# Optimization experiments

Measured on AMD Instinct MI355X. Metric: run time of the kernel, lower is better.

Reference implementation:

```python
import jax, jax.numpy as jnp
import numpy as np

N_PAIRS = 100000
N_TRIP = 500000
PAIR_DIM = 128
GEOM_DIM = 4


def _mlp(x, w1, b1, w2, b2):
    return jax.nn.silu(x @ w1 + b1) @ w2 + b2


def setup_inputs() -> dict:
    key = jax.random.key(0)
    ks = jax.random.split(key, 16)

    def lin(k, fan_in, fan_out):
        bound = 1.0 / np.sqrt(fan_in)
        kw, kb = jax.random.split(k)
        w = jax.random.uniform(kw, (fan_in, fan_out), jnp.float32, -bound, bound)
        b = jax.random.uniform(kb, (fan_out,), jnp.float32, -bound, bound)
        return w, b

    psi_w1, psi_b1 = lin(ks[0], 3 * PAIR_DIM + GEOM_DIM, PAIR_DIM)
    psi_w2, psi_b2 = lin(ks[1], PAIR_DIM, PAIR_DIM)
    phi_w1, phi_b1 = lin(ks[2], 2 * PAIR_DIM, PAIR_DIM)
    phi_w2, phi_b2 = lin(ks[3], PAIR_DIM, PAIR_DIM)

    return {
        "h_pair": jax.random.normal(ks[4], (N_PAIRS, PAIR_DIM), jnp.float32),
        "pair_vu_idx": jax.random.randint(ks[5], (N_TRIP,), 0, N_PAIRS, jnp.int64 if jax.config.jax_enable_x64 else jnp.int32).astype(jnp.int32),
        "pair_uw_idx": jax.random.randint(ks[6], (N_TRIP,), 0, N_PAIRS).astype(jnp.int32),
        "pair_vw_idx": jax.random.randint(ks[7], (N_TRIP,), 0, N_PAIRS).astype(jnp.int32),
        "geom_features": jax.random.normal(ks[8], (N_TRIP, GEOM_DIM), jnp.float32),
        "psi_w1": psi_w1, "psi_b1": psi_b1, "psi_w2": psi_w2, "psi_b2": psi_b2,
        "phi_w1": phi_w1, "phi_b1": phi_b1, "phi_w2": phi_w2, "phi_b2": phi_b2,
    }


def reference(h_pair, pair_vu_idx, pair_uw_idx, pair_vw_idx, geom_features,
              psi_w1, psi_b1, psi_w2, psi_b2,
              phi_w1, phi_b1, phi_w2, phi_b2):
    # gather triplet endpoints: [T, pair_dim] each
    h_vu = h_pair[pair_vu_idx]
    h_uw = h_pair[pair_uw_idx]
    h_vw = h_pair[pair_vw_idx]
    triplet_input = jnp.concatenate([h_vu, h_uw, h_vw, geom_features], axis=-1)  # [T, 3D+G]
    m_triplet = _mlp(triplet_input, psi_w1, psi_b1, psi_w2, psi_b2)  # [T, D]
    # scatter-add back onto pairs indexed by vw
    agg = jax.ops.segment_sum(m_triplet, pair_vw_idx, num_segments=h_pair.shape[0])  # [N, D]
    updated = _mlp(jnp.concatenate([h_pair, agg], axis=-1), phi_w1, phi_b1, phi_w2, phi_b2)
    return h_pair + updated
```

## Files before the change

### kernel.cpp

```cpp
#include <hip/hip_runtime.h>
#include <hip/hip_bf16.h>

#define T_TRIP 500000
#define NP     100000
#define NTILES 7813

typedef float f32x4 __attribute__((ext_vector_type(4)));
typedef __bf16 bf16x8 __attribute__((ext_vector_type(8)));
typedef unsigned short u16;
typedef unsigned short u16x8 __attribute__((ext_vector_type(8)));

__device__ __forceinline__ u16 f2bf(float f) {
  union { float f; unsigned u; } v; v.f = f;
  unsigned r = v.u + 0x7fffu + ((v.u >> 16) & 1u);
  return (u16)(r >> 16);
}

__device__ __forceinline__ ushort4 cvt4(float4 v) {
  ushort4 o; o.x = f2bf(v.x); o.y = f2bf(v.y); o.z = f2bf(v.z); o.w = f2bf(v.w);
  return o;
}

__device__ __forceinline__ u16 cvt1_pk(float v) {
  unsigned r;
  asm("v_cvt_pk_bf16_f32 %0, %1, %1" : "=v"(r) : "v"(v));
  return (u16)r;
}

#define MFMA16(a, b, c) __builtin_amdgcn_mfma_f32_16x16x32_bf16((a), (b), (c), 0, 0, 0)

#define WAITVM(N) asm volatile("s_waitcnt vmcnt(" #N ")" ::: "memory")
#define LGKM0()   asm volatile("s_waitcnt lgkmcnt(0)" ::: "memory")

__device__ __forceinline__ void barrier_raw() {
  asm volatile("" ::: "memory");
  __builtin_amdgcn_s_barrier();
  asm volatile("" ::: "memory");
  __builtin_amdgcn_sched_barrier(0);
}

__device__ __forceinline__ void gload_lds16(const u16* g, u16* l) {
  __builtin_amdgcn_global_load_lds((const __attribute__((address_space(1))) void*)g,
                                   (__attribute__((address_space(3))) void*)l, 16, 0, 0);
}
__device__ __forceinline__ void gload_lds4(const int* g, int* l) {
  __builtin_amdgcn_global_load_lds((const __attribute__((address_space(1))) void*)g,
                                   (__attribute__((address_space(3))) void*)l, 4, 0, 0);
}

#define FP_W1A   0u
#define FP_W1B   16384u
#define FP_W1C   32768u
#define FP_W2    49152u
#define FP_PW1   65536u
#define FP_PW2   98304u
#define FP_W1D   114688u
#define FP_H     131072u
#define FP_AGG   12931072u
#define WS_NEED_BYTES 51462144ull

#define HSTR  136
#define GSTR  520
#define X2STR 264

__global__ void k_prep_fast(const float* __restrict__ psi_w1, const float* __restrict__ psi_w2,
                            const float* __restrict__ phi_w1, const float* __restrict__ phi_w2,
                            u16* __restrict__ ws) {
  int i = blockIdx.x * 256 + threadIdx.x;
  if (i < 49152) {
    int s = i / 16384, r = i % 16384;
    int n = r / 128, k = r % 128;
    ws[FP_W1A + i] = f2bf(psi_w1[(s * 128 + k) * 128 + n]);
    return;
  }
  i -= 49152;
  if (i < 16384) {
    int n = i / 128, k = i % 128;
    ws[FP_W2 + i] = f2bf(psi_w2[k * 128 + n]);
    return;
  }
  i -= 16384;
  if (i < 32768) {
    int n = i / 256, k = i % 256;
    ws[FP_PW1 + i] = f2bf(phi_w1[k * 128 + n]);
    return;
  }
  i -= 32768;
  if (i < 16384) {
    int n = i / 128, k = i % 128;
    ws[FP_PW2 + i] = f2bf(phi_w2[k * 128 + n]);
    return;
  }
  i -= 16384;
  if (i < 512) {
    int k = i / 128, n = i % 128;
    reinterpret_cast<float*>(ws + FP_W1D)[i] = psi_w1[(384 + k) * 128 + n];
  }
}

__global__ void k_hconv(const float* __restrict__ h, u16* __restrict__ H, u16* __restrict__ AGG) {
  const size_t i = (size_t)(blockIdx.x * 256 + threadIdx.x) * 8;
  float4 v0 = *reinterpret_cast<const float4*>(h + i);
  float4 v1 = *reinterpret_cast<const float4*>(h + i + 4);
  *reinterpret_cast<ushort4*>(H + i)     = cvt4(v0);
  *reinterpret_cast<ushort4*>(H + i + 4) = cvt4(v1);
  ushort4 z = {0, 0, 0, 0};
  *reinterpret_cast<ushort4*>(AGG + i)     = z;
  *reinterpret_cast<ushort4*>(AGG + i + 4) = z;
}

__global__ __launch_bounds__(256, 3) void k_triplet_fast(
    const u16* __restrict__ H,
    const int* __restrict__ ivu, const int* __restrict__ iuw, const int* __restrict__ ivw,
    const float* __restrict__ geom,
    const u16* __restrict__ W1A, const u16* __restrict__ W1B, const u16* __restrict__ W1C,
    const float* __restrict__ w1dF, const u16* __restrict__ W2T,
    const float* __restrict__ b1, const float* __restrict__ b2,
    u16* __restrict__ AGG) {
  __shared__ __align__(16) u16 XB[2][16 * GSTR];
  __shared__ __align__(16) u16 hl[64 * HSTR];
  __shared__ __align__(16) float geomF[64][4];
  __shared__ __align__(16) int aIvu[2][64];
  __shared__ __align__(16) int aIuw[64];
  __shared__ __align__(16) int svw[2][64];

  const int tid = threadIdx.x;
  const int w = tid >> 6, l = tid & 63;
  const int lr = l & 15;
  const int lk = (l >> 4) << 3;
  const int n0 = w * 32 + lr;
  const int rowh = (l >> 4) << 2;
  const int srow = l >> 4;
  const int schunk = (l & 15) ^ ((l >> 4) << 1);

  bf16x8 w2f[4][2];
#pragma unroll
  for (int ks = 0; ks < 4; ++ks)
#pragma unroll
    for (int ct = 0; ct < 2; ++ct)
      w2f[ks][ct] = *reinterpret_cast<const bf16x8*>(&W2T[(size_t)(n0 + ct * 16) * 128 + ks * 32 + lk]);
  const float b1v[2] = {b1[n0], b1[n0 + 16]};
  const float b2v[2] = {b2[n0], b2[n0 + 16]};
  float w1dv[4][2];
#pragma unroll
  for (int k = 0; k < 4; ++k) {
    w1dv[k][0] = w1dF[k * 128 + n0];
    w1dv[k][1] = w1dF[k * 128 + n0 + 16];
  }

  auto stage_src_lds = [&](const int* idxL, int buf) {
#pragma unroll
    for (int q = 0; q < 4; ++q) {
      const int g = w * 4 + q;
      const int idx = idxL[g * 4 + srow];
      gload_lds16(H + (size_t)idx * 128 + schunk * 8, &XB[buf][g * GSTR]);
    }
  };

  auto stage_aux = [&](int tn, int tn2, int buf) {
    if (w == 0) {
      int t = tn2 * 64 + l; t = (t < T_TRIP) ? t : (T_TRIP - 1);
      gload_lds4(ivu + t, &aIvu[buf][0]);
    } else if (w == 1) {
      int t = tn * 64 + l; t = (t < T_TRIP) ? t : (T_TRIP - 1);
      gload_lds4(iuw + t, &aIuw[0]);
    } else if (w == 2) {
      int t = tn * 64 + l; t = (t < T_TRIP) ? t : (T_TRIP - 1);
      gload_lds4(ivw + t, &svw[buf][0]);
    } else {
      int t = tn * 64 + l; t = (t < T_TRIP) ? t : (T_TRIP - 1);
      gload_lds16(reinterpret_cast<const u16*>(geom + (size_t)t * 4),
                  reinterpret_cast<u16*>(&geomF[0][0]));
    }
  };

  auto gemm_src = [&](const u16* WT, int buf, f32x4 (&acc)[4][2]) {
#pragma unroll
    for (int ks = 0; ks < 4; ++ks) {
      bf16x8 a[4], b[2];
#pragma unroll
      for (int rt = 0; rt < 4; ++rt) {
        const int r = rt * 16 + lr;
        const int g = r >> 2, s = r & 3;
        const int j = ks * 4 + (l >> 4);
        a[rt] = *reinterpret_cast<const bf16x8*>(&XB[buf][g * GSTR + s * 128 + ((j ^ (s << 1)) << 3)]);
      }
#pragma unroll
      for (int ct = 0; ct < 2; ++ct)
        b[ct] = *reinterpret_cast<const bf16x8*>(&WT[(size_t)(n0 + ct * 16) * 128 + ks * 32 + lk]);
#pragma unroll
      for (int rt = 0; rt < 4; ++rt)
#pragma unroll
        for (int ct = 0; ct < 2; ++ct)
          acc[rt][ct] = MFMA16(a[rt], b[ct], acc[rt][ct]);
    }
  };

  int4 dst4[4];
  f32x4 acc2c[4][2];
#pragma unroll
  for (int rt = 0; rt < 4; ++rt) {
    dst4[rt] = make_int4(-1, -1, -1, -1);
#pragma unroll
    for (int ct = 0; ct < 2; ++ct) acc2c[rt][ct] = f32x4{0.f, 0.f, 0.f, 0.f};
  }

  auto scatter_prev = [&]() {
#pragma unroll
    for (int rt = 0; rt < 4; ++rt) {
#pragma unroll
      for (int j = 0; j < 4; ++j) {
        const int dst = (&dst4[rt].x)[j];
        float v0 = acc2c[rt][0][j];
        float v1 = acc2c[rt][1][j];
        float x0 = __shfl_xor(v0, 1);
        float x1 = __shfl_xor(v1, 1);
        const bool even = (l & 1) == 0;
        float lo = even ? v0 : x1;
        float hi = even ? x0 : v1;
        const int col = even ? n0 : (n0 + 15);
        if (dst >= 0) {
          u16* p = AGG + (size_t)dst * 128 + col;
          unsigned pk;
          asm("v_cvt_pk_bf16_f32 %0, %1, %2" : "=v"(pk) : "v"(lo), "v"(hi));
          asm volatile("global_atomic_pk_add_bf16 %0, %1, off" :: "v"(p), "v"(pk) : "memory");
        }
      }
    }
  };

  int pb = 0, tb = 0;
  int tt = blockIdx.x;
  const int G = gridDim.x;

  {
    int tn2 = (tt + G < NTILES) ? tt + G : tt;
    stage_aux(tt, tn2, 0);
#pragma unroll
    for (int q = 0; q < 4; ++q) {
      const int g = w * 4 + q;
      int t = tt * 64 + g * 4 + srow; t = (t < T_TRIP) ? t : (T_TRIP - 1);
      const int idx = ivu[t];
      gload_lds16(H + (size_t)idx * 128 + schunk * 8, &XB[0][g * GSTR]);
    }
    WAITVM(0);
    barrier_raw();
  }

  for (; tt < NTILES; tt += G) {
    const int t0 = tt * 64;

    stage_src_lds(aIuw, pb ^ 1);
    WAITVM(4);
    barrier_raw();

    f32x4 acc[4][2] = {};
    gemm_src(W1A, pb, acc);
    barrier_raw();

    int4 nd[4];
#pragma unroll
    for (int rt = 0; rt < 4; ++rt)
      nd[rt] = *reinterpret_cast<const int4*>(&svw[tb][rt * 16 + rowh]);
    stage_src_lds(&svw[tb][0], pb);
    WAITVM(4);
    barrier_raw();

    gemm_src(W1B, pb ^ 1, acc);
    WAITVM(0);
    barrier_raw();

    stage_src_lds(&aIvu[tb][0], pb ^ 1);

    gemm_src(W1C, pb, acc);

    scatter_prev();

#pragma unroll
    for (int rt = 0; rt < 4; ++rt)
#pragma unroll
      for (int j = 0; j < 4; ++j) {
        const float4 g4 = *reinterpret_cast<const float4*>(&geomF[rt * 16 + rowh + j][0]);
#pragma unroll
        for (int ct = 0; ct < 2; ++ct)
          acc[rt][ct][j] += g4.x * w1dv[0][ct] + g4.y * w1dv[1][ct] +
                            g4.z * w1dv[2][ct] + g4.w * w1dv[3][ct];
      }
#pragma unroll
    for (int rt = 0; rt < 4; ++rt)
#pragma unroll
      for (int ct = 0; ct < 2; ++ct) {
        const float bb = b1v[ct];
#pragma unroll
        for (int j = 0; j < 4; ++j) {
          float v = acc[rt][ct][j] + bb;
          v = v * __builtin_amdgcn_rcpf(1.f + __expf(-v));
          hl[(rt * 16 + rowh + j) * HSTR + n0 + ct * 16] = cvt1_pk(v);
        }
      }
    LGKM0();
    barrier_raw();

    {
      int tn = (tt + G < NTILES) ? tt + G : tt;
      int tn2 = (tt + 2 * G < NTILES) ? tt + 2 * G : tt;
      stage_aux(tn, tn2, tb ^ 1);
    }

    f32x4 acc2[4][2] = {};
#pragma unroll
    for (int ks = 0; ks < 4; ++ks) {
      bf16x8 a[4];
#pragma unroll
      for (int rt = 0; rt < 4; ++rt)
        a[rt] = *reinterpret_cast<const bf16x8*>(&hl[(rt * 16 + lr) * HSTR + ks * 32 + lk]);
#pragma unroll
      for (int rt = 0; rt < 4; ++rt)
#pragma unroll
        for (int ct = 0; ct < 2; ++ct)
          acc2[rt][ct] = MFMA16(a[rt], w2f[ks][ct], acc2[rt][ct]);
    }

#pragma unroll
    for (int rt = 0; rt < 4; ++rt) {
#pragma unroll
      for (int j = 0; j < 4; ++j) {
        const int trow = t0 + rt * 16 + rowh + j;
        (&dst4[rt].x)[j] = (trow < T_TRIP) ? (&nd[rt].x)[j] : -1;
      }
#pragma unroll
      for (int ct = 0; ct < 2; ++ct)
        acc2c[rt][ct] = acc2[rt][ct] + b2v[ct];
    }

    WAITVM(0);
    barrier_raw();
    pb ^= 1; tb ^= 1;
  }

  scatter_prev();
  WAITVM(0);
}

__global__ __launch_bounds__(256, 3) void k_pair_fast(
    const float* __restrict__ h_pair, const u16* __restrict__ H, const u16* __restrict__ AGG,
    const u16* __restrict__ PW1T, const u16* __restrict__ PW2T,
    const float* __restrict__ b1, const float* __restrict__ b2,
    float* __restrict__ out) {
  __shared__ __align__(16) u16 xl[64 * X2STR];
  __shared__ __align__(16) u16 hl[64 * HSTR];

  const int tid = threadIdx.x;
  const int r0 = blockIdx.x * 64;

  {
    const int row = tid >> 2, q = tid & 3;
    int rc = r0 + row; rc = (rc < NP) ? rc : (NP - 1);
    const u16x8* sh = reinterpret_cast<const u16x8*>(H + (size_t)rc * 128 + q * 32);
    const u16x8* sa = reinterpret_cast<const u16x8*>(AGG + (size_t)rc * 128 + q * 32);
    u16x8* d1 = reinterpret_cast<u16x8*>(&xl[row * X2STR + q * 32]);
    u16x8* d2 = reinterpret_cast<u16x8*>(&xl[row * X2STR + 128 + q * 32]);
#pragma unroll
    for (int i = 0; i < 4; ++i) { d1[i] = sh[i]; d2[i] = sa[i]; }
  }
  __syncthreads();

  const int w = tid >> 6, l = tid & 63;
  const int lr = l & 15;
  const int lk = (l >> 4) << 3;
  const int n0 = w * 32 + lr;
  const int rowh = (l >> 4) << 2;

  f32x4 acc[4][2] = {};
#pragma unroll 1
  for (int ks = 0; ks < 8; ++ks) {
    const int k0 = ks * 32;
    bf16x8 a[4], b[2];
#pragma unroll
    for (int rt = 0; rt < 4; ++rt)
      a[rt] = *reinterpret_cast<const bf16x8*>(&xl[(rt * 16 + lr) * X2STR + k0 + lk]);
#pragma unroll
    for (int ct = 0; ct < 2; ++ct)
      b[ct] = *reinterpret_cast<const bf16x8*>(&PW1T[(size_t)(n0 + ct * 16) * 256 + k0 + lk]);
#pragma unroll
    for (int rt = 0; rt < 4; ++rt)
#pragma unroll
      for (int ct = 0; ct < 2; ++ct)
        acc[rt][ct] = MFMA16(a[rt], b[ct], acc[rt][ct]);
  }

  {
    const float b1v0 = b1[n0], b1v1 = b1[n0 + 16];
#pragma unroll
    for (int rt = 0; rt < 4; ++rt)
#pragma unroll
      for (int ct = 0; ct < 2; ++ct) {
        const float bb = ct ? b1v1 : b1v0;
#pragma unroll
        for (int j = 0; j < 4; ++j) {
          float v = acc[rt][ct][j] + bb;
          v = v * __builtin_amdgcn_rcpf(1.f + __expf(-v));
          hl[(rt * 16 + rowh + j) * HSTR + n0 + ct * 16] = cvt1_pk(v);
        }
      }
  }
  __syncthreads();

  f32x4 acc2[4][2] = {};
#pragma unroll
  for (int ks = 0; ks < 4; ++ks) {
    const int k0 = ks * 32;
    bf16x8 a[4], b[2];
#pragma unroll
    for (int rt = 0; rt < 4; ++rt)
      a[rt] = *reinterpret_cast<const bf16x8*>(&hl[(rt * 16 + lr) * HSTR + k0 + lk]);
#pragma unroll
    for (int ct = 0; ct < 2; ++ct)
      b[ct] = *reinterpret_cast<const bf16x8*>(&PW2T[(size_t)(n0 + ct * 16) * 128 + k0 + lk]);
#pragma unroll
    for (int rt = 0; rt < 4; ++rt)
#pragma unroll
      for (int ct = 0; ct < 2; ++ct)
        acc2[rt][ct] = MFMA16(a[rt], b[ct], acc2[rt][ct]);
  }

  {
    const float b2v0 = b2[n0], b2v1 = b2[n0 + 16];
#pragma unroll
    for (int rt = 0; rt < 4; ++rt)
#pragma unroll
      for (int j = 0; j < 4; ++j) {
        const int row = rt * 16 + rowh + j;
        const int r = r0 + row;
        if (r < NP) {
          out[(size_t)r * 128 + n0]      = h_pair[(size_t)r * 128 + n0]      + acc2[rt][0][j] + b2v0;
          out[(size_t)r * 128 + n0 + 16] = h_pair[(size_t)r * 128 + n0 + 16] + acc2[rt][1][j] + b2v1;
        }
      }
  }
}

#define PSI_W1T_OFF 0
#define PSI_W2T_OFF 53248
#define PHI_W1T_OFF 69632
#define PHI_W2T_OFF 102400
#define WS_U16_TOTAL 118784
#define XSTR 424

__global__ void k_prep(const float* __restrict__ psi_w1, const float* __restrict__ psi_w2,
                       const float* __restrict__ phi_w1, const float* __restrict__ phi_w2,
                       u16* __restrict__ ws) {
  int i = blockIdx.x * 256 + threadIdx.x;
  if (i < 128 * 416) {
    int n = i / 416, k = i % 416;
    ws[PSI_W1T_OFF + i] = f2bf(k < 388 ? psi_w1[k * 128 + n] : 0.f);
    return;
  }
  i -= 128 * 416;
  if (i < 128 * 128) {
    int n = i / 128, k = i % 128;
    ws[PSI_W2T_OFF + i] = f2bf(psi_w2[k * 128 + n]);
    return;
  }
  i -= 128 * 128;
  if (i < 128 * 256) {
    int n = i / 256, k = i % 256;
    ws[PHI_W1T_OFF + i] = f2bf(phi_w1[k * 128 + n]);
    return;
  }
  i -= 128 * 256;
  if (i < 128 * 128) {
    int n = i / 128, k = i % 128;
    ws[PHI_W2T_OFF + i] = f2bf(phi_w2[k * 128 + n]);
  }
}

__global__ __launch_bounds__(256, 2) void k_triplet(
    const float* __restrict__ h_pair,
    const int* __restrict__ ivu, const int* __restrict__ iuw, const int* __restrict__ ivw,
    const float* __restrict__ geom,
    const u16* __restrict__ W1T, const u16* __restrict__ W2T,
    const float* __restrict__ b1, const float* __restrict__ b2,
    float* __restrict__ agg) {
  __shared__ __align__(16) u16 xl[64 * XSTR];
  __shared__ __align__(16) u16 hl[64 * HSTR];
  __shared__ int svw[64];

  const int tid = threadIdx.x;
  const int t0 = blockIdx.x * 64;

  {
    const int row = tid >> 2, q = tid & 3;
    const int t = t0 + row;
    const int tc = (t < T_TRIP) ? t : (T_TRIP - 1);
    if (q == 0) svw[row] = (t < T_TRIP) ? ivw[tc] : -1;
    int idx[3];
    idx[0] = ivu[tc]; idx[1] = iuw[tc]; idx[2] = ivw[tc];
#pragma unroll
    for (int s = 0; s < 3; ++s) {
      const float4* src = reinterpret_cast<const float4*>(h_pair + (size_t)idx[s] * 128 + q * 32);
      u16* dst = &xl[row * XSTR + s * 128 + q * 32];
#pragma unroll
      for (int i = 0; i < 8; ++i)
        *reinterpret_cast<ushort4*>(dst + i * 4) = cvt4(src[i]);
    }
  }
  if (tid < 64) {
    const int t = t0 + tid;
    const int tc = (t < T_TRIP) ? t : (T_TRIP - 1);
    const float4 g = reinterpret_cast<const float4*>(geom)[tc];
    u16* dst = &xl[tid * XSTR + 384];
    *reinterpret_cast<ushort4*>(dst) = cvt4(g);
    ushort4 z = {0, 0, 0, 0};
#pragma unroll
    for (int i = 1; i < 8; ++i) *reinterpret_cast<ushort4*>(dst + i * 4) = z;
  }
  __syncthreads();

  const int w = tid >> 6;
  const int l = tid & 63;
  const int lr = l & 15;
  const int lk = (l >> 4) << 3;
  const int n0 = w * 32 + lr;
  const int rowh = (l >> 4) << 2;

  f32x4 acc[4][2] = {};
#pragma unroll 1
  for (int ks = 0; ks < 13; ++ks) {
    const int k0 = ks * 32;
    bf16x8 a[4], b[2];
#pragma unroll
    for (int rt = 0; rt < 4; ++rt)
      a[rt] = *reinterpret_cast<const bf16x8*>(&xl[(rt * 16 + lr) * XSTR + k0 + lk]);
#pragma unroll
    for (int ct = 0; ct < 2; ++ct)
      b[ct] = *reinterpret_cast<const bf16x8*>(&W1T[(size_t)(n0 + ct * 16) * 416 + k0 + lk]);
#pragma unroll
    for (int rt = 0; rt < 4; ++rt)
#pragma unroll
      for (int ct = 0; ct < 2; ++ct)
        acc[rt][ct] = MFMA16(a[rt], b[ct], acc[rt][ct]);
  }

  {
    const float b1v0 = b1[n0], b1v1 = b1[n0 + 16];
#pragma unroll
    for (int rt = 0; rt < 4; ++rt)
#pragma unroll
      for (int ct = 0; ct < 2; ++ct) {
        const float bb = ct ? b1v1 : b1v0;
#pragma unroll
        for (int j = 0; j < 4; ++j) {
          float v = acc[rt][ct][j] + bb;
          v = v / (1.f + __expf(-v));
          hl[(rt * 16 + rowh + j) * HSTR + n0 + ct * 16] = f2bf(v);
        }
      }
  }
  __syncthreads();

  f32x4 acc2[4][2] = {};
#pragma unroll
  for (int ks = 0; ks < 4; ++ks) {
    const int k0 = ks * 32;
    bf16x8 a[4], b[2];
#pragma unroll
    for (int rt = 0; rt < 4; ++rt)
      a[rt] = *reinterpret_cast<const bf16x8*>(&hl[(rt * 16 + lr) * HSTR + k0 + lk]);
#pragma unroll
    for (int ct = 0; ct < 2; ++ct)
      b[ct] = *reinterpret_cast<const bf16x8*>(&W2T[(size_t)(n0 + ct * 16) * 128 + k0 + lk]);
#pragma unroll
    for (int rt = 0; rt < 4; ++rt)
#pragma unroll
      for (int ct = 0; ct < 2; ++ct)
        acc2[rt][ct] = MFMA16(a[rt], b[ct], acc2[rt][ct]);
  }

  {
    const float b2v0 = b2[n0], b2v1 = b2[n0 + 16];
#pragma unroll
    for (int rt = 0; rt < 4; ++rt)
#pragma unroll
      for (int j = 0; j < 4; ++j) {
        const int row = rt * 16 + rowh + j;
        const int dst = svw[row];
        if (dst >= 0) {
          unsafeAtomicAdd(&agg[(size_t)dst * 128 + n0], acc2[rt][0][j] + b2v0);
          unsafeAtomicAdd(&agg[(size_t)dst * 128 + n0 + 16], acc2[rt][1][j] + b2v1);
        }
      }
  }
}

__global__ __launch_bounds__(256, 2) void k_pair(
    const float* __restrict__ h_pair,
    const u16* __restrict__ W1T, const u16* __restrict__ W2T,
    const float* __restrict__ b1, const float* __restrict__ b2,
    float* __restrict__ out) {
  __shared__ __align__(16) u16 xl[64 * X2STR];
  __shared__ __align__(16) u16 hl[64 * HSTR];

  const int tid = threadIdx.x;
  const int r0 = blockIdx.x * 64;

  {
    const int row = tid >> 2, q = tid & 3;
    const int r = r0 + row;
    const int rc = (r < NP) ? r : (NP - 1);
    const float4* s1 = reinterpret_cast<const float4*>(h_pair + (size_t)rc * 128 + q * 32);
    const float4* s2 = reinterpret_cast<const float4*>(out + (size_t)rc * 128 + q * 32);
    u16* d1 = &xl[row * X2STR + q * 32];
    u16* d2 = &xl[row * X2STR + 128 + q * 32];
#pragma unroll
    for (int i = 0; i < 8; ++i) {
      *reinterpret_cast<ushort4*>(d1 + i * 4) = cvt4(s1[i]);
      *reinterpret_cast<ushort4*>(d2 + i * 4) = cvt4(s2[i]);
    }
  }
  __syncthreads();

  const int w = tid >> 6;
  const int l = tid & 63;
  const int lr = l & 15;
  const int lk = (l >> 4) << 3;
  const int n0 = w * 32 + lr;
  const int rowh = (l >> 4) << 2;

  f32x4 acc[4][2] = {};
#pragma unroll 1
  for (int ks = 0; ks < 8; ++ks) {
    const int k0 = ks * 32;
    bf16x8 a[4], b[2];
#pragma unroll
    for (int rt = 0; rt < 4; ++rt)
      a[rt] = *reinterpret_cast<const bf16x8*>(&xl[(rt * 16 + lr) * X2STR + k0 + lk]);
#pragma unroll
    for (int ct = 0; ct < 2; ++ct)
      b[ct] = *reinterpret_cast<const bf16x8*>(&W1T[(size_t)(n0 + ct * 16) * 256 + k0 + lk]);
#pragma unroll
    for (int rt = 0; rt < 4; ++rt)
#pragma unroll
      for (int ct = 0; ct < 2; ++ct)
        acc[rt][ct] = MFMA16(a[rt], b[ct], acc[rt][ct]);
  }

  {
    const float b1v0 = b1[n0], b1v1 = b1[n0 + 16];
#pragma unroll
    for (int rt = 0; rt < 4; ++rt)
#pragma unroll
      for (int ct = 0; ct < 2; ++ct) {
        const float bb = ct ? b1v1 : b1v0;
#pragma unroll
        for (int j = 0; j < 4; ++j) {
          float v = acc[rt][ct][j] + bb;
          v = v / (1.f + __expf(-v));
          hl[(rt * 16 + rowh + j) * HSTR + n0 + ct * 16] = f2bf(v);
        }
      }
  }
  __syncthreads();

  f32x4 acc2[4][2] = {};
#pragma unroll
  for (int ks = 0; ks < 4; ++ks) {
    const int k0 = ks * 32;
    bf16x8 a[4], b[2];
#pragma unroll
    for (int rt = 0; rt < 4; ++rt)
      a[rt] = *reinterpret_cast<const bf16x8*>(&hl[(rt * 16 + lr) * HSTR + k0 + lk]);
#pragma unroll
    for (int ct = 0; ct < 2; ++ct)
      b[ct] = *reinterpret_cast<const bf16x8*>(&W2T[(size_t)(n0 + ct * 16) * 128 + k0 + lk]);
#pragma unroll
    for (int rt = 0; rt < 4; ++rt)
#pragma unroll
      for (int ct = 0; ct < 2; ++ct)
        acc2[rt][ct] = MFMA16(a[rt], b[ct], acc2[rt][ct]);
  }

  {
    const float b2v0 = b2[n0], b2v1 = b2[n0 + 16];
#pragma unroll
    for (int rt = 0; rt < 4; ++rt)
#pragma unroll
      for (int j = 0; j < 4; ++j) {
        const int row = rt * 16 + rowh + j;
        const int r = r0 + row;
        if (r < NP) {
          out[(size_t)r * 128 + n0]      = h_pair[(size_t)r * 128 + n0]      + acc2[rt][0][j] + b2v0;
          out[(size_t)r * 128 + n0 + 16] = h_pair[(size_t)r * 128 + n0 + 16] + acc2[rt][1][j] + b2v1;
        }
      }
  }
}

extern "C" void kernel_launch(void* const* d_in, const int* in_sizes, int n_in,
                              void* d_out, int out_size, void* d_ws, size_t ws_size,
                              hipStream_t stream) {
  const float* h_pair = (const float*)d_in[0];
  const int* ivu = (const int*)d_in[1];
  const int* iuw = (const int*)d_in[2];
  const int* ivw = (const int*)d_in[3];
  const float* geom = (const float*)d_in[4];
  const float* psi_w1 = (const float*)d_in[5];
  const float* psi_b1 = (const float*)d_in[6];
  const float* psi_w2 = (const float*)d_in[7];
  const float* psi_b2 = (const float*)d_in[8];
  const float* phi_w1 = (const float*)d_in[9];
  const float* phi_b1 = (const float*)d_in[10];
  const float* phi_w2 = (const float*)d_in[11];
  const float* phi_b2 = (const float*)d_in[12];

  float* out = (float*)d_out;
  u16* ws = (u16*)d_ws;

  if (ws_size >= WS_NEED_BYTES) {
    k_prep_fast<<<450, 256, 0, stream>>>(psi_w1, psi_w2, phi_w1, phi_w2, ws);
    k_hconv<<<6250, 256, 0, stream>>>(h_pair, ws + FP_H, ws + FP_AGG);
    k_triplet_fast<<<768, 256, 0, stream>>>(
        ws + FP_H, ivu, iuw, ivw, geom,
        ws + FP_W1A, ws + FP_W1B, ws + FP_W1C,
        reinterpret_cast<const float*>(ws + FP_W1D), ws + FP_W2,
        psi_b1, psi_b2, ws + FP_AGG);
    k_pair_fast<<<(NP + 63) / 64, 256, 0, stream>>>(
        h_pair, ws + FP_H, ws + FP_AGG,
        ws + FP_PW1, ws + FP_PW2, phi_b1, phi_b2, out);
  } else {
    hipMemsetAsync(d_out, 0, (size_t)out_size * sizeof(float), stream);
    k_prep<<<(WS_U16_TOTAL + 255) / 256, 256, 0, stream>>>(psi_w1, psi_w2, phi_w1, phi_w2, ws);
    k_triplet<<<(T_TRIP + 63) / 64, 256, 0, stream>>>(
        h_pair, ivu, iuw, ivw, geom,
        ws + PSI_W1T_OFF, ws + PSI_W2T_OFF, psi_b1, psi_b2, out);
    k_pair<<<(NP + 63) / 64, 256, 0, stream>>>(
        h_pair, ws + PHI_W1T_OFF, ws + PHI_W2T_OFF, phi_b1, phi_b2, out);
  }
}
```

Before: 299.3 us.

## Sort triplets by destination pair and replace atomic scatter with pull reduction

Adds a counting sort of triplets by their vw index (histogram, three-stage scan, atomic-cursor permutation), after which the triplet MLP writes per-triplet messages in bf16 to a dense buffer instead of issuing bf16 atomic adds. The pair kernel then sums each pair's contiguous message range before its MLP, so the scatter becomes segmented and contention-free. This trades the atomic traffic for several extra launches, a message buffer of about 128 MB written and read back, and a serial per-pair summation loop. The path only runs when the workspace is large enough. The old fast triplet kernel is also reworked to load indices directly rather than staging them in LDS.

New measurement: 408.7 us. 1.37x slower.

```diff
diff --git a/kernel.cpp b/kernel.cpp
--- a/kernel.cpp
+++ b/kernel.cpp
@@ -4,11 +4,13 @@
 #define T_TRIP 500000
 #define NP     100000
 #define NTILES 7813
+#define NPAD   500032
 
 typedef float f32x4 __attribute__((ext_vector_type(4)));
 typedef __bf16 bf16x8 __attribute__((ext_vector_type(8)));
 typedef unsigned short u16;
 typedef unsigned short u16x8 __attribute__((ext_vector_type(8)));
+typedef unsigned int u32;
 
 __device__ __forceinline__ u16 f2bf(float f) {
   union { float f; unsigned u; } v; v.f = f;
@@ -25,6 +27,13 @@
   unsigned r;
   asm("v_cvt_pk_bf16_f32 %0, %1, %1" : "=v"(r) : "v"(v));
   return (u16)r;
+}
+
+__device__ __forceinline__ float bflo(u32 d) {
+  union { u32 u; float f; } v; v.u = d << 16; return v.f;
+}
+__device__ __forceinline__ float bfhi(u32 d) {
+  union { u32 u; float f; } v; v.u = d & 0xffff0000u; return v.f;
 }
 
 #define MFMA16(a, b, c) __builtin_amdgcn_mfma_f32_16x16x32_bf16((a), (b), (c), 0, 0, 0)
@@ -59,6 +68,17 @@
 #define FP_AGG   12931072u
 #define WS_NEED_BYTES 51462144ull
 
+#define FP_M_BYTE 25862144ull
+#define SB_CNT    153870336ull
+#define SB_START  154270464ull
+#define SB_CURSOR 154670592ull
+#define SB_BSUM   155070720ull
+#define SB_IVU    155071232ull
+#define SB_IUW    157071360ull
+#define SB_IVW    159071488ull
+#define SB_GEOM   161071616ull
+#define WS_SORT_BYTES 169072128ull
+
 #define HSTR  136
 #define GSTR  520
 #define X2STR 264
@@ -107,6 +127,397 @@
   ushort4 z = {0, 0, 0, 0};
   *reinterpret_cast<ushort4*>(AGG + i)     = z;
   *reinterpret_cast<ushort4*>(AGG + i + 4) = z;
+}
+
+__global__ void k_hconv2(const float* __restrict__ h, u16* __restrict__ H) {
+  const size_t i = (size_t)(blockIdx.x * 256 + threadIdx.x) * 8;
+  float4 v0 = *reinterpret_cast<const float4*>(h + i);
+  float4 v1 = *reinterpret_cast<const float4*>(h + i + 4);
+  *reinterpret_cast<ushort4*>(H + i)     = cvt4(v0);
+  *reinterpret_cast<ushort4*>(H + i + 4) = cvt4(v1);
+}
+
+__global__ void k_hist(const int* __restrict__ ivw, int* __restrict__ cnt) {
+  int i = blockIdx.x * 256 + threadIdx.x;
+  if (i < T_TRIP) atomicAdd(&cnt[ivw[i]], 1);
+}
+
+__global__ __launch_bounds__(1024) void k_scan1(const int* __restrict__ cnt,
+                                                int* __restrict__ tmp, int* __restrict__ bsum) {
+  __shared__ int wsum[16];
+  const int idx = blockIdx.x * 1024 + threadIdx.x;
+  const int lane = threadIdx.x & 63, wid = threadIdx.x >> 6;
+  int v = (idx < NP) ? cnt[idx] : 0;
+  int x = v;
+#pragma unroll
+  for (int off = 1; off < 64; off <<= 1) {
+    int n = __shfl_up(x, off);
+    if (lane >= off) x += n;
+  }
+  if (lane == 63) wsum[wid] = x;
+  __syncthreads();
+  if (threadIdx.x < 16) {
+    int s = wsum[threadIdx.x];
+#pragma unroll
+    for (int off = 1; off < 16; off <<= 1) {
+      int n = __shfl_up(s, off);
+      if (threadIdx.x >= off) s += n;
+    }
+    wsum[threadIdx.x] = s;
+  }
+  __syncthreads();
+  const int base = wid ? wsum[wid - 1] : 0;
+  if (idx < NP) tmp[idx] = base + x - v;
+  if (threadIdx.x == 1023) bsum[blockIdx.x] = base + x;
+}
+
+__global__ void k_scan2(int* __restrict__ bsum) {
+  __shared__ int s[128];
+  const int t = threadIdx.x;
+  int v = (t < 98) ? bsum[t] : 0;
+  s[t] = v; __syncthreads();
+#pragma unroll
+  for (int off = 1; off < 128; off <<= 1) {
+    int a = (t >= off) ? s[t - off] : 0;
+    __syncthreads();
+    s[t] += a;
+    __syncthreads();
+  }
+  if (t < 98) bsum[t] = s[t] - v;
+}
+
+__global__ void k_scan3(const int* __restrict__ bsum, int* __restrict__ start,
+                        int* __restrict__ cursor) {
+  int idx = blockIdx.x * 256 + threadIdx.x;
+  if (idx < NP) {
+    int f = start[idx] + bsum[idx >> 10];
+    start[idx] = f;
+    cursor[idx] = f;
+  }
+  if (idx == 0) start[NP] = T_TRIP;
+}
+
+__global__ void k_perm(const int* __restrict__ ivu, const int* __restrict__ iuw,
+                       const int* __restrict__ ivw, const float* __restrict__ geom,
+                       int* __restrict__ cursor,
+                       int* __restrict__ ivu_s, int* __restrict__ iuw_s,
+                       int* __restrict__ ivw_s, float4* __restrict__ geom_s) {
+  int i = blockIdx.x * 256 + threadIdx.x;
+  if (i < T_TRIP) {
+    int v = ivw[i];
+    int pos = atomicAdd(&cursor[v], 1);
+    ivu_s[pos] = ivu[i];
+    iuw_s[pos] = iuw[i];
+    ivw_s[pos] = v;
+    geom_s[pos] = reinterpret_cast<const float4*>(geom)[i];
+  } else if (i < NPAD) {
+    ivu_s[i] = 0; iuw_s[i] = 0; ivw_s[i] = 0;
+    geom_s[i] = make_float4(0.f, 0.f, 0.f, 0.f);
+  }
+}
+
+__global__ __launch_bounds__(256, 3) void k_triplet_sorted(
+    const u16* __restrict__ H,
+    const int* __restrict__ ivu_s, const int* __restrict__ iuw_s, const int* __restrict__ ivw_s,
+    const float* __restrict__ geom_s,
+    const u16* __restrict__ W1A, const u16* __restrict__ W1B, const u16* __restrict__ W1C,
+    const float* __restrict__ w1dF, const u16* __restrict__ W2T,
+    const float* __restrict__ b1, const float* __restrict__ b2,
+    u32* __restrict__ M32) {
+  __shared__ __align__(16) u16 XB[2][16 * GSTR];
+  __shared__ __align__(16) u16 hl[64 * HSTR];
+  __shared__ __align__(16) float geomF[64][4];
+  __shared__ __align__(16) int aIvu[2][64];
+  __shared__ __align__(16) int aIuw[64];
+  __shared__ __align__(16) int aIvw[64];
+
+  const int tid = threadIdx.x;
+  const int w = tid >> 6, l = tid & 63;
+  const int lr = l & 15;
+  const int lk = (l >> 4) << 3;
+  const int n0 = w * 32 + lr;
+  const int rowh = (l >> 4) << 2;
+  const int srow = l >> 4;
+  const int schunk = (l & 15) ^ ((l >> 4) << 1);
+
+  bf16x8 w2f[4][2];
+#pragma unroll
+  for (int ks = 0; ks < 4; ++ks)
+#pragma unroll
+    for (int ct = 0; ct < 2; ++ct)
+      w2f[ks][ct] = *reinterpret_cast<const bf16x8*>(&W2T[(size_t)(n0 + ct * 16) * 128 + ks * 32 + lk]);
+  const float b1v[2] = {b1[n0], b1[n0 + 16]};
+  const float b2v[2] = {b2[n0], b2[n0 + 16]};
+  float w1dv[4][2];
+#pragma unroll
+  for (int k = 0; k < 4; ++k) {
+    w1dv[k][0] = w1dF[k * 128 + n0];
+    w1dv[k][1] = w1dF[k * 128 + n0 + 16];
+  }
+
+  auto stage_src_lds = [&](const int* idxL, int buf) {
+#pragma unroll
+    for (int q = 0; q < 4; ++q) {
+      const int g = w * 4 + q;
+      const int idx = idxL[g * 4 + srow];
+      gload_lds16(H + (size_t)idx * 128 + schunk * 8, &XB[buf][g * GSTR]);
+    }
+  };
+
+  auto stage_aux = [&](int tA, int tB, int buf) {
+    if (w == 0) {
+      gload_lds4(ivu_s + tB * 64 + l, &aIvu[buf][0]);
+    } else if (w == 1) {
+      gload_lds4(iuw_s + tA * 64 + l, &aIuw[0]);
+    } else if (w == 2) {
+      gload_lds4(ivw_s + tA * 64 + l, &aIvw[0]);
+    } else {
+      gload_lds16(reinterpret_cast<const u16*>(geom_s + (size_t)(tA * 64 + l) * 4),
+                  reinterpret_cast<u16*>(&geomF[0][0]));
+    }
+  };
+
+  auto gemm_src = [&](const u16* WT, int buf, f32x4 (&acc)[4][2]) {
+#pragma unroll
+    for (int ks = 0; ks < 4; ++ks) {
+      bf16x8 a[4], b[2];
+#pragma unroll
+      for (int rt = 0; rt < 4; ++rt) {
+        const int r = rt * 16 + lr;
+        const int g = r >> 2, s = r & 3;
+        const int j = ks * 4 + (l >> 4);
+        a[rt] = *reinterpret_cast<const bf16x8*>(&XB[buf][g * GSTR + s * 128 + ((j ^ (s << 1)) << 3)]);
+      }
+#pragma unroll
+      for (int ct = 0; ct < 2; ++ct)
+        b[ct] = *reinterpret_cast<const bf16x8*>(&WT[(size_t)(n0 + ct * 16) * 128 + ks * 32 + lk]);
+#pragma unroll
+      for (int rt = 0; rt < 4; ++rt)
+#pragma unroll
+        for (int ct = 0; ct < 2; ++ct)
+          acc[rt][ct] = MFMA16(a[rt], b[ct], acc[rt][ct]);
+    }
+  };
+
+  int pb = 0, tb = 0;
+  int tt = blockIdx.x;
+  const int G = gridDim.x;
+
+  {
+    int tB = (tt + G < NTILES) ? tt + G : NTILES - 1;
+    stage_aux(tt, tB, 0);
+#pragma unroll
+    for (int q = 0; q < 4; ++q) {
+      const int g = w * 4 + q;
+      const int t = tt * 64 + g * 4 + srow;
+      const int idx = ivu_s[t];
+      gload_lds16(H + (size_t)idx * 128 + schunk * 8, &XB[0][g * GSTR]);
+    }
+    WAITVM(0);
+    barrier_raw();
+  }
+
+  for (; tt < NTILES; tt += G) {
+    const int t0 = tt * 64;
+
+    stage_src_lds(aIuw, pb ^ 1);
+    f32x4 acc[4][2] = {};
+    gemm_src(W1A, pb, acc);
+    barrier_raw();
+
+    stage_src_lds(aIvw, pb);
+    WAITVM(4);
+    barrier_raw();
+
+    gemm_src(W1B, pb ^ 1, acc);
+    WAITVM(0);
+    barrier_raw();
+
+    stage_src_lds(&aIvu[tb][0], pb ^ 1);
+    gemm_src(W1C, pb, acc);
+
+#pragma unroll
+    for (int rt = 0; rt < 4; ++rt)
+#pragma unroll
+      for (int j = 0; j < 4; ++j) {
+        const float4 g4 = *reinterpret_cast<const float4*>(&geomF[rt * 16 + rowh + j][0]);
+#pragma unroll
+        for (int ct = 0; ct < 2; ++ct)
+          acc[rt][ct][j] += g4.x * w1dv[0][ct] + g4.y * w1dv[1][ct] +
+                            g4.z * w1dv[2][ct] + g4.w * w1dv[3][ct];
+      }
+#pragma unroll
+    for (int rt = 0; rt < 4; ++rt)
+#pragma unroll
+      for (int ct = 0; ct < 2; ++ct) {
+        const float bb = b1v[ct];
+#pragma unroll
+        for (int j = 0; j < 4; ++j) {
+          float v = acc[rt][ct][j] + bb;
+          v = v * __builtin_amdgcn_rcpf(1.f + __expf(-v));
+          hl[(rt * 16 + rowh + j) * HSTR + n0 + ct * 16] = cvt1_pk(v);
+        }
+      }
+    LGKM0();
+    barrier_raw();
+
+    {
+      int tA = (tt + G < NTILES) ? tt + G : NTILES - 1;
+      int tB = (tt + 2 * G < NTILES) ? tt + 2 * G : NTILES - 1;
+      stage_aux(tA, tB, tb ^ 1);
+    }
+
+    f32x4 acc2[4][2] = {};
+#pragma unroll
+    for (int ks = 0; ks < 4; ++ks) {
+      bf16x8 a[4];
+#pragma unroll
+      for (int rt = 0; rt < 4; ++rt)
+        a[rt] = *reinterpret_cast<const bf16x8*>(&hl[(rt * 16 + lr) * HSTR + ks * 32 + lk]);
+#pragma unroll
+      for (int rt = 0; rt < 4; ++rt)
+#pragma unroll
+        for (int ct = 0; ct < 2; ++ct)
+          acc2[rt][ct] = MFMA16(a[rt], w2f[ks][ct], acc2[rt][ct]);
+    }
+
+#pragma unroll
+    for (int rt = 0; rt < 4; ++rt)
+#pragma unroll
+      for (int j = 0; j < 4; ++j) {
+        float v0 = acc2[rt][0][j] + b2v[0];
+        float v1 = acc2[rt][1][j] + b2v[1];
+        float x0 = __shfl_xor(v0, 1);
+        float x1 = __shfl_xor(v1, 1);
+        const bool even = (l & 1) == 0;
+        float lo = even ? v0 : x1;
+        float hi = even ? x0 : v1;
+        const int dcol = even ? (n0 >> 1) : ((n0 + 15) >> 1);
+        u32 pk;
+        asm("v_cvt_pk_bf16_f32 %0, %1, %2" : "=v"(pk) : "v"(lo), "v"(hi));
+        const int row = t0 + rt * 16 + rowh + j;
+        M32[(size_t)row * 64 + dcol] = pk;
+      }
+
+    WAITVM(16);
+    barrier_raw();
+    pb ^= 1; tb ^= 1;
+  }
+  WAITVM(0);
+}
+
+__global__ __launch_bounds__(256, 3) void k_pair_pull(
+    const float* __restrict__ h_pair, const u16* __restrict__ H,
+    const u32* __restrict__ M32, const int* __restrict__ start,
+    const u16* __restrict__ PW1T, const u16* __restrict__ PW2T,
+    const float* __restrict__ b1, const float* __restrict__ b2,
+    float* __restrict__ out) {
+  __shared__ __align__(16) u16 xl[64 * X2STR];
+  __shared__ __align__(16) u16 hl[64 * HSTR];
+
+  const int tid = threadIdx.x;
+  const int r0 = blockIdx.x * 64;
+
+  {
+    const int row = tid >> 2, q = tid & 3;
+    int rc = r0 + row; rc = (rc < NP) ? rc : (NP - 1);
+    const u16x8* sh = reinterpret_cast<const u16x8*>(H + (size_t)rc * 128 + q * 32);
+    u16x8* d1 = reinterpret_cast<u16x8*>(&xl[row * X2STR + q * 32]);
+#pragma unroll
+    for (int i = 0; i < 4; ++i) d1[i] = sh[i];
+  }
+
+  const int w = tid >> 6, l = tid & 63;
+  u32* xl32 = reinterpret_cast<u32*>(xl);
+
+  for (int i = 0; i < 16; ++i) {
+    int p = r0 + w * 16 + i;
+    int pc = (p < NP) ? p : (NP - 1);
+    const int s = start[pc], e = start[pc + 1];
+    float lo = 0.f, hi = 0.f;
+    for (int r = s; r < e; ++r) {
+      u32 d = M32[(size_t)r * 64 + l];
+      lo += bflo(d);
+      hi += bfhi(d);
+    }
+    u32 pk;
+    asm("v_cvt_pk_bf16_f32 %0, %1, %2" : "=v"(pk) : "v"(lo), "v"(hi));
+    xl32[(w * 16 + i) * (X2STR / 2) + 64 + l] = pk;
+  }
+  __syncthreads();
+
+  const int lr = l & 15;
+  const int lk = (l >> 4) << 3;
+  const int n0 = w * 32 + lr;
+  const int rowh = (l >> 4) << 2;
+
+  f32x4 acc[4][2] = {};
+#pragma unroll 1
+  for (int ks = 0; ks < 8; ++ks) {
+    const int k0 = ks * 32;
+    bf16x8 a[4], b[2];
+#pragma unroll
+    for (int rt = 0; rt < 4; ++rt)
+      a[rt] = *reinterpret_cast<const bf16x8*>(&xl[(rt * 16 + lr) * X2STR + k0 + lk]);
+#pragma unroll
+    for (int ct = 0; ct < 2; ++ct)
+      b[ct] = *reinterpret_cast<const bf16x8*>(&PW1T[(size_t)(n0 + ct * 16) * 256 + k0 + lk]);
+#pragma unroll
+    for (int rt = 0; rt < 4; ++rt)
+#pragma unroll
+      for (int ct = 0; ct < 2; ++ct)
+        acc[rt][ct] = MFMA16(a[rt], b[ct], acc[rt][ct]);
+  }
+
+  {
+    const float b1v0 = b1[n0], b1v1 = b1[n0 + 16];
+#pragma unroll
+    for (int rt = 0; rt < 4; ++rt)
+#pragma unroll
+      for (int ct = 0; ct < 2; ++ct) {
+        const float bb = ct ? b1v1 : b1v0;
+#pragma unroll
+        for (int j = 0; j < 4; ++j) {
+          float v = acc[rt][ct][j] + bb;
+          v = v * __builtin_amdgcn_rcpf(1.f + __expf(-v));
+          hl[(rt * 16 + rowh + j) * HSTR + n0 + ct * 16] = cvt1_pk(v);
+        }
+      }
+  }
+  __syncthreads();
+
+  f32x4 acc2[4][2] = {};
+#pragma unroll
+  for (int ks = 0; ks < 4; ++ks) {
+    const int k0 = ks * 32;
+    bf16x8 a[4], b[2];
+#pragma unroll
+    for (int rt = 0; rt < 4; ++rt)
+      a[rt] = *reinterpret_cast<const bf16x8*>(&hl[(rt * 16 + lr) * HSTR + k0 + lk]);
+#pragma unroll
+    for (int ct = 0; ct < 2; ++ct)
+      b[ct] = *reinterpret_cast<const bf16x8*>(&PW2T[(size_t)(n0 + ct * 16) * 128 + k0 + lk]);
+#pragma unroll
+    for (int rt = 0; rt < 4; ++rt)
+#pragma unroll
+      for (int ct = 0; ct < 2; ++ct)
+        acc2[rt][ct] = MFMA16(a[rt], b[ct], acc2[rt][ct]);
+  }
+
+  {
+    const float b2v0 = b2[n0], b2v1 = b2[n0 + 16];
+#pragma unroll
+    for (int rt = 0; rt < 4; ++rt)
+#pragma unroll
+      for (int j = 0; j < 4; ++j) {
+        const int row = rt * 16 + rowh + j;
+        const int r = r0 + row;
+        if (r < NP) {
+          out[(size_t)r * 128 + n0]      = h_pair[(size_t)r * 128 + n0]      + acc2[rt][0][j] + b2v0;
+          out[(size_t)r * 128 + n0 + 16] = h_pair[(size_t)r * 128 + n0 + 16] + acc2[rt][1][j] + b2v1;
+        }
+      }
+  }
 }
 
 __global__ __launch_bounds__(256, 3) void k_triplet_fast(
@@ -119,10 +530,8 @@
     u16* __restrict__ AGG) {
   __shared__ __align__(16) u16 XB[2][16 * GSTR];
   __shared__ __align__(16) u16 hl[64 * HSTR];
-  __shared__ __align__(16) float geomF[64][4];
-  __shared__ __align__(16) int aIvu[2][64];
-  __shared__ __align__(16) int aIuw[64];
-  __shared__ __align__(16) int svw[2][64];
+  __shared__ __align__(16) float geomF[2][64][4];
+  __shared__ int svw[2][64];
 
   const int tid = threadIdx.x;
   const int w = tid >> 6, l = tid & 63;
@@ -148,29 +557,24 @@
     w1dv[k][1] = w1dF[k * 128 + n0 + 16];
   }
 
-  auto stage_src_lds = [&](const int* idxL, int buf) {
+  auto stage_src = [&](const int* idxa, int tile, int buf) {
+    const int t0 = tile * 64;
 #pragma unroll
     for (int q = 0; q < 4; ++q) {
       const int g = w * 4 + q;
-      const int idx = idxL[g * 4 + srow];
+      int t = t0 + g * 4 + srow; t = (t < T_TRIP) ? t : (T_TRIP - 1);
+      const int idx = idxa[t];
       gload_lds16(H + (size_t)idx * 128 + schunk * 8, &XB[buf][g * GSTR]);
     }
   };
 
-  auto stage_aux = [&](int tn, int tn2, int buf) {
+  auto stage_aux = [&](int tile, int tb2) {
+    int t = tile * 64 + l; t = (t < T_TRIP) ? t : (T_TRIP - 1);
     if (w == 0) {
-      int t = tn2 * 64 + l; t = (t < T_TRIP) ? t : (T_TRIP - 1);
-      gload_lds4(ivu + t, &aIvu[buf][0]);
+      gload_lds16(reinterpret_cast<const u16*>(geom + (size_t)t * 4),
+                  reinterpret_cast<u16*>(&geomF[tb2][0][0]));
     } else if (w == 1) {
-      int t = tn * 64 + l; t = (t < T_TRIP) ? t : (T_TRIP - 1);
-      gload_lds4(iuw + t, &aIuw[0]);
-    } else if (w == 2) {
-      int t = tn * 64 + l; t = (t < T_TRIP) ? t : (T_TRIP - 1);
-      gload_lds4(ivw + t, &svw[buf][0]);
-    } else {
-      int t = tn * 64 + l; t = (t < T_TRIP) ? t : (T_TRIP - 1);
-      gload_lds16(reinterpret_cast<const u16*>(geom + (size_t)t * 4),
-                  reinterpret_cast<u16*>(&geomF[0][0]));
+      gload_lds4(ivw + t, &svw[tb2][0]);
     }
   };
 
@@ -196,149 +600,103 @@
     }
   };
 
-  int4 dst4[4];
-  f32x4 acc2c[4][2];
-#pragma unroll
-  for (int rt = 0; rt < 4; ++rt) {
-    dst4[rt] = make_int4(-1, -1, -1, -1);
-#pragma unroll
-    for (int ct = 0; ct < 2; ++ct) acc2c[rt][ct] = f32x4{0.f, 0.f, 0.f, 0.f};
-  }
-
-  auto scatter_prev = [&]() {
+  int pb = 0, tb = 0;
+  int tt = blockIdx.x;
+  stage_src(ivu, tt, 0);
+
+  for (; tt < NTILES; tt += gridDim.x) {
+    const int t0 = tt * 64;
+    int ttn = tt + gridDim.x; if (ttn >= NTILES) ttn = tt;
+
+    stage_src(iuw, tt, pb ^ 1);
+    stage_aux(tt, tb);
+    WAITVM(4);
+    barrier_raw();
+
+    f32x4 acc[4][2] = {};
+    gemm_src(W1A, pb, acc);
+    barrier_raw();
+
+    stage_src(ivw, tt, pb);
+    WAITVM(4);
+    barrier_raw();
+
+    gemm_src(W1B, pb ^ 1, acc);
+    WAITVM(0);
+    barrier_raw();
+
+    stage_src(ivu, ttn, pb ^ 1);
+    gemm_src(W1C, pb, acc);
+
+#pragma unroll
+    for (int rt = 0; rt < 4; ++rt)
+#pragma unroll
+      for (int j = 0; j < 4; ++j) {
+        const float4 g4 = *reinterpret_cast<const float4*>(&geomF[tb][rt * 16 + rowh + j][0]);
+#pragma unroll
+        for (int ct = 0; ct < 2; ++ct)
+          acc[rt][ct][j] += g4.x * w1dv[0][ct] + g4.y * w1dv[1][ct] +
+                            g4.z * w1dv[2][ct] + g4.w * w1dv[3][ct];
+      }
+#pragma unroll
+    for (int rt = 0; rt < 4; ++rt)
+#pragma unroll
+      for (int ct = 0; ct < 2; ++ct) {
+        const float bb = b1v[ct];
+#pragma unroll
+        for (int j = 0; j < 4; ++j) {
+          float v = acc[rt][ct][j] + bb;
+          v = v * __builtin_amdgcn_rcpf(1.f + __expf(-v));
+          hl[(rt * 16 + rowh + j) * HSTR + n0 + ct * 16] = cvt1_pk(v);
+        }
+      }
+    LGKM0();
+    barrier_raw();
+
+    {
+      int tn = tt + gridDim.x; if (tn >= NTILES) tn = tt;
+      stage_aux(tn, tb ^ 1);
+    }
+
+    f32x4 acc2[4][2] = {};
+#pragma unroll
+    for (int ks = 0; ks < 4; ++ks) {
+      bf16x8 a[4];
+#pragma unroll
+      for (int rt = 0; rt < 4; ++rt)
+        a[rt] = *reinterpret_cast<const bf16x8*>(&hl[(rt * 16 + lr) * HSTR + ks * 32 + lk]);
+#pragma unroll
+      for (int rt = 0; rt < 4; ++rt)
+#pragma unroll
+        for (int ct = 0; ct < 2; ++ct)
+          acc2[rt][ct] = MFMA16(a[rt], w2f[ks][ct], acc2[rt][ct]);
+    }
+
 #pragma unroll
     for (int rt = 0; rt < 4; ++rt) {
+      const int4 d4 = *reinterpret_cast<const int4*>(&svw[tb][rt * 16 + rowh]);
 #pragma unroll
       for (int j = 0; j < 4; ++j) {
-        const int dst = (&dst4[rt].x)[j];
-        float v0 = acc2c[rt][0][j];
-        float v1 = acc2c[rt][1][j];
+        const int dst = (&d4.x)[j];
+        const int trow = t0 + rt * 16 + rowh + j;
+        float v0 = acc2[rt][0][j] + b2v[0];
+        float v1 = acc2[rt][1][j] + b2v[1];
         float x0 = __shfl_xor(v0, 1);
         float x1 = __shfl_xor(v1, 1);
         const bool even = (l & 1) == 0;
         float lo = even ? v0 : x1;
         float hi = even ? x0 : v1;
         const int col = even ? n0 : (n0 + 15);
-        if (dst >= 0) {
+        if (trow < T_TRIP) {
           u16* p = AGG + (size_t)dst * 128 + col;
-          unsigned pk;
+          u32 pk;
           asm("v_cvt_pk_bf16_f32 %0, %1, %2" : "=v"(pk) : "v"(lo), "v"(hi));
           asm volatile("global_atomic_pk_add_bf16 %0, %1, off" :: "v"(p), "v"(pk) : "memory");
         }
       }
     }
-  };
-
-  int pb = 0, tb = 0;
-  int tt = blockIdx.x;
-  const int G = gridDim.x;
-
-  {
-    int tn2 = (tt + G < NTILES) ? tt + G : tt;
-    stage_aux(tt, tn2, 0);
-#pragma unroll
-    for (int q = 0; q < 4; ++q) {
-      const int g = w * 4 + q;
-      int t = tt * 64 + g * 4 + srow; t = (t < T_TRIP) ? t : (T_TRIP - 1);
-      const int idx = ivu[t];
-      gload_lds16(H + (size_t)idx * 128 + schunk * 8, &XB[0][g * GSTR]);
-    }
-    WAITVM(0);
-    barrier_raw();
-  }
-
-  for (; tt < NTILES; tt += G) {
-    const int t0 = tt * 64;
-
-    stage_src_lds(aIuw, pb ^ 1);
-    WAITVM(4);
-    barrier_raw();
-
-    f32x4 acc[4][2] = {};
-    gemm_src(W1A, pb, acc);
-    barrier_raw();
-
-    int4 nd[4];
-#pragma unroll
-    for (int rt = 0; rt < 4; ++rt)
-      nd[rt] = *reinterpret_cast<const int4*>(&svw[tb][rt * 16 + rowh]);
-    stage_src_lds(&svw[tb][0], pb);
-    WAITVM(4);
-    barrier_raw();
-
-    gemm_src(W1B, pb ^ 1, acc);
-    WAITVM(0);
-    barrier_raw();
-
-    stage_src_lds(&aIvu[tb][0], pb ^ 1);
-
-    gemm_src(W1C, pb, acc);
-
-    scatter_prev();
-
-#pragma unroll
-    for (int rt = 0; rt < 4; ++rt)
-#pragma unroll
-      for (int j = 0; j < 4; ++j) {
-        const float4 g4 = *reinterpret_cast<const float4*>(&geomF[rt * 16 + rowh + j][0]);
-#pragma unroll
-        for (int ct = 0; ct < 2; ++ct)
-          acc[rt][ct][j] += g4.x * w1dv[0][ct] + g4.y * w1dv[1][ct] +
-                            g4.z * w1dv[2][ct] + g4.w * w1dv[3][ct];
-      }
-#pragma unroll
-    for (int rt = 0; rt < 4; ++rt)
-#pragma unroll
-      for (int ct = 0; ct < 2; ++ct) {
-        const float bb = b1v[ct];
-#pragma unroll
-        for (int j = 0; j < 4; ++j) {
-          float v = acc[rt][ct][j] + bb;
-          v = v * __builtin_amdgcn_rcpf(1.f + __expf(-v));
-          hl[(rt * 16 + rowh + j) * HSTR + n0 + ct * 16] = cvt1_pk(v);
-        }
-      }
-    LGKM0();
-    barrier_raw();
-
-    {
-      int tn = (tt + G < NTILES) ? tt + G : tt;
-      int tn2 = (tt + 2 * G < NTILES) ? tt + 2 * G : tt;
-      stage_aux(tn, tn2, tb ^ 1);
-    }
-
-    f32x4 acc2[4][2] = {};
-#pragma unroll
-    for (int ks = 0; ks < 4; ++ks) {
-      bf16x8 a[4];
-#pragma unroll
-      for (int rt = 0; rt < 4; ++rt)
-        a[rt] = *reinterpret_cast<const bf16x8*>(&hl[(rt * 16 + lr) * HSTR + ks * 32 + lk]);
-#pragma unroll
-      for (int rt = 0; rt < 4; ++rt)
-#pragma unroll
-        for (int ct = 0; ct < 2; ++ct)
-          acc2[rt][ct] = MFMA16(a[rt], w2f[ks][ct], acc2[rt][ct]);
-    }
-
-#pragma unroll
-    for (int rt = 0; rt < 4; ++rt) {
-#pragma unroll
-      for (int j = 0; j < 4; ++j) {
-        const int trow = t0 + rt * 16 + rowh + j;
-        (&dst4[rt].x)[j] = (trow < T_TRIP) ? (&nd[rt].x)[j] : -1;
-      }
-#pragma unroll
-      for (int ct = 0; ct < 2; ++ct)
-        acc2c[rt][ct] = acc2[rt][ct] + b2v[ct];
-    }
-
-    WAITVM(0);
-    barrier_raw();
     pb ^= 1; tb ^= 1;
   }
-
-  scatter_prev();
   WAITVM(0);
 }
 
@@ -715,8 +1073,37 @@
 
   float* out = (float*)d_out;
   u16* ws = (u16*)d_ws;
-
-  if (ws_size >= WS_NEED_BYTES) {
+  char* wsb = (char*)d_ws;
+
+  if (ws_size >= WS_SORT_BYTES) {
+    u32*  M32    = (u32*)(wsb + FP_M_BYTE);
+    int*  cnt    = (int*)(wsb + SB_CNT);
+    int*  start  = (int*)(wsb + SB_START);
+    int*  cursor = (int*)(wsb + SB_CURSOR);
+    int*  bsum   = (int*)(wsb + SB_BSUM);
+    int*  ivu_s  = (int*)(wsb + SB_IVU);
+    int*  iuw_s  = (int*)(wsb + SB_IUW);
+    int*  ivw_s  = (int*)(wsb + SB_IVW);
+    float4* geom_s = (float4*)(wsb + SB_GEOM);
+
+    k_prep_fast<<<450, 256, 0, stream>>>(psi_w1, psi_w2, phi_w1, phi_w2, ws);
+    k_hconv2<<<6250, 256, 0, stream>>>(h_pair, ws + FP_H);
+    hipMemsetAsync(cnt, 0, NP * sizeof(int), stream);
+    k_hist<<<(T_TRIP + 255) / 256, 256, 0, stream>>>(ivw, cnt);
+    k_scan1<<<98, 1024, 0, stream>>>(cnt, start, bsum);
+    k_scan2<<<1, 128, 0, stream>>>(bsum);
+    k_scan3<<<(NP + 255) / 256, 256, 0, stream>>>(bsum, start, cursor);
+    k_perm<<<(NPAD + 255) / 256, 256, 0, stream>>>(ivu, iuw, ivw, geom, cursor,
+                                                   ivu_s, iuw_s, ivw_s, geom_s);
+    k_triplet_sorted<<<768, 256, 0, stream>>>(
+        ws + FP_H, ivu_s, iuw_s, ivw_s, (const float*)geom_s,
+        ws + FP_W1A, ws + FP_W1B, ws + FP_W1C,
+        reinterpret_cast<const float*>(ws + FP_W1D), ws + FP_W2,
+        psi_b1, psi_b2, M32);
+    k_pair_pull<<<(NP + 63) / 64, 256, 0, stream>>>(
+        h_pair, ws + FP_H, M32, start,
+        ws + FP_PW1, ws + FP_PW2, phi_b1, phi_b2, out);
+  } else if (ws_size >= WS_NEED_BYTES) {
     k_prep_fast<<<450, 256, 0, stream>>>(psi_w1, psi_w2, phi_w1, phi_w2, ws);
     k_hconv<<<6250, 256, 0, stream>>>(h_pair, ws + FP_H, ws + FP_AGG);
     k_triplet_fast<<<768, 256, 0, stream>>>(
```
